# Kernel tuning notes

Hardware: AMD Instinct MI355X
Metric: run time of the kernel (lower is better)

Reference implementation:

```python
import jax, jax.numpy as jnp
import numpy as np

EPS = 1e-6        # RMSNorm epsilon (LLaMA convention)
THETA = 10000.0   # RoPE base, from eqx.nn.RotaryPositionalEmbedding(head_dim, 10000)


def rms_norm(x, w):
    # x: [seq, d]; w: [d]
    var = jnp.mean(x * x, axis=-1, keepdims=True)
    return x * jax.lax.rsqrt(var + EPS) * w


def rope(x, offset):
    # x: [seq, heads, head_dim]; half-split (NeoX/equinox) rotation
    seq, _, hd = x.shape
    half = hd // 2
    inv_freq = 1.0 / (THETA ** (jnp.arange(0, half, dtype=jnp.float32) * 2.0 / hd))
    pos = jnp.arange(seq, dtype=jnp.float32) + offset
    ang = jnp.outer(pos, inv_freq)              # [seq, half]
    cos = jnp.cos(ang)[:, None, :]              # [seq, 1, half]
    sin = jnp.sin(ang)[:, None, :]
    x1, x2 = x[..., :half], x[..., half:]
    return jnp.concatenate([x1 * cos - x2 * sin, x2 * cos + x1 * sin], axis=-1)


def setup_inputs() -> dict:
    D, H, HD, S, C = 4096, 32, 128, 1024, 2048
    ks = jax.random.split(jax.random.key(0), 7)
    sc = 1.0 / np.sqrt(D).astype(np.float32)
    return {
        "xs": jax.random.normal(ks[0], (S, D), jnp.float32),
        "cache_k": jax.random.normal(ks[1], (C, H, HD), jnp.float32),
        "cache_v": jax.random.normal(ks[2], (C, H, HD), jnp.float32),
        "norm_w": jnp.ones((D,), jnp.float32),
        "wq": jax.random.normal(ks[3], (D, D), jnp.float32) * sc,
        "wk": jax.random.normal(ks[4], (D, D), jnp.float32) * sc,
        "wv": jax.random.normal(ks[5], (D, D), jnp.float32) * sc,
        "wo": jax.random.normal(ks[6], (D, D), jnp.float32) * sc,
    }


def reference(xs, cache_k, cache_v, norm_w, wq, wk, wv, wo):
    S, D = xs.shape
    C, H, HD = cache_k.shape
    xn = rms_norm(xs, norm_w)                                   # [S, D]
    # eqx.nn.Linear stores weight as [out, in]: y = x @ W.T
    q = rope((xn @ wq.T).reshape(S, H, HD), C)                  # [S, H, HD]
    k_new = rope((xn @ wk.T).reshape(S, H, HD), C)
    v_new = (xn @ wv.T).reshape(S, H, HD)
    k = jnp.concatenate([cache_k, k_new], axis=0)               # [C+S, H, HD]
    v = jnp.concatenate([cache_v, v_new], axis=0)
    scores = jnp.einsum('shd,thd->hst', q, k) / np.float32(np.sqrt(HD))
    # causal with KV cache: query i (global pos C+i) attends keys j <= C+i
    mask = jnp.arange(C + S)[None, :] <= (jnp.arange(S)[:, None] + C)
    scores = jnp.where(mask[None, :, :], scores, jnp.float32(-1e30))
    probs = jax.nn.softmax(scores, axis=-1)                     # [H, S, C+S]
    attn = jnp.einsum('hst,thd->shd', probs, v).reshape(S, D)
    return attn @ wo.T                                          # [S, D]
```

## Files before the change

kernel.cpp:

```cpp
#include <hip/hip_runtime.h>
#include <cmath>

#define S_LEN 1024
#define D_DIM 4096
#define H_NUM 32
#define HD_DIM 128
#define C_LEN 2048
#define T_LEN 3072

using u16 = unsigned short;
typedef __bf16 bf16x8 __attribute__((ext_vector_type(8)));
typedef float f32x4 __attribute__((ext_vector_type(4)));

__device__ __forceinline__ u16 f2bf(float f) {
  unsigned u = __float_as_uint(f);
  return (u16)((u + 0x7FFFu + ((u >> 16) & 1u)) >> 16);
}

__device__ __forceinline__ f32x4 mfma16(bf16x8 a, bf16x8 b, f32x4 c) {
  return __builtin_amdgcn_mfma_f32_16x16x32_bf16(a, b, c, 0, 0, 0);
}

__device__ __forceinline__ void async_cp16(const u16* g, u16* l) {
  __builtin_amdgcn_global_load_lds((const __attribute__((address_space(1))) unsigned int*)g,
                                   (__attribute__((address_space(3))) unsigned int*)l,
                                   16, 0, 0);
}

__global__ __launch_bounds__(256) void cvt_w4(const float* __restrict__ w0, const float* __restrict__ w1,
                                              const float* __restrict__ w2, const float* __restrict__ w3,
                                              u16* __restrict__ dst) {
  int y = blockIdx.y;
  const float* src = (y == 0) ? w0 : (y == 1) ? w1 : (y == 2) ? w2 : w3;
  int i = blockIdx.x * 256 + threadIdx.x;
  float4 v = ((const float4*)src)[i];
  ushort4 o;
  o.x = f2bf(v.x); o.y = f2bf(v.y); o.z = f2bf(v.z); o.w = f2bf(v.w);
  ((ushort4*)(dst + (size_t)y * D_DIM * D_DIM))[i] = o;
}

__global__ __launch_bounds__(256) void rmsnorm_k(const float* __restrict__ xs, const float* __restrict__ w,
                                                 u16* __restrict__ xn) {
  int row = blockIdx.x, tid = threadIdx.x;
  const float* xr = xs + (size_t)row * D_DIM;
  float4 xv[4];
  float ss = 0.f;
#pragma unroll
  for (int g = 0; g < 4; ++g) {
    xv[g] = *(const float4*)(xr + g * 1024 + tid * 4);
    ss += xv[g].x * xv[g].x + xv[g].y * xv[g].y + xv[g].z * xv[g].z + xv[g].w * xv[g].w;
  }
#pragma unroll
  for (int m = 1; m < 64; m <<= 1) ss += __shfl_xor(ss, m);
  __shared__ float red[4];
  if ((tid & 63) == 0) red[tid >> 6] = ss;
  __syncthreads();
  float rs = rsqrtf((red[0] + red[1] + red[2] + red[3]) * (1.f / D_DIM) + 1e-6f);
  u16* xo = xn + (size_t)row * D_DIM;
#pragma unroll
  for (int g = 0; g < 4; ++g) {
    float4 wv = *(const float4*)(w + g * 1024 + tid * 4);
    ushort4 o;
    o.x = f2bf(xv[g].x * rs * wv.x);
    o.y = f2bf(xv[g].y * rs * wv.y);
    o.z = f2bf(xv[g].z * rs * wv.z);
    o.w = f2bf(xv[g].w * rs * wv.w);
    *(ushort4*)(xo + g * 1024 + tid * 4) = o;
  }
}

__global__ __launch_bounds__(256) void gemm_bt(const u16* __restrict__ A,
                                               const u16* __restrict__ B0, const u16* __restrict__ B1,
                                               const u16* __restrict__ B2,
                                               float* __restrict__ C0, float* __restrict__ C1,
                                               float* __restrict__ C2) {
  __shared__ u16 As[2 * 128 * 32];
  __shared__ u16 Bs[2 * 128 * 32];
  int tid = threadIdx.x;
  int wave = tid >> 6, lane = tid & 63, quad = lane >> 4, l15 = lane & 15;
  int wm = wave >> 1, wn = wave & 1;
  int m0 = blockIdx.y * 128, n0 = blockIdx.x * 128;
  int bz = blockIdx.z;
  const u16* Bp = (bz == 0) ? B0 : ((bz == 1) ? B1 : B2);
  float* Cp = (bz == 0) ? C0 : ((bz == 1) ? C1 : C2);

  f32x4 acc[4][4];
  const f32x4 zero4 = {0.f, 0.f, 0.f, 0.f};
#pragma unroll
  for (int mt = 0; mt < 4; ++mt)
#pragma unroll
    for (int nt = 0; nt < 4; ++nt) acc[mt][nt] = zero4;

  int ar = tid >> 2, acol = (tid & 3) * 8;
  const u16* ga0 = A + (size_t)(m0 + ar) * D_DIM + acol;
  const u16* ga1 = A + (size_t)(m0 + 64 + ar) * D_DIM + acol;
  const u16* gb0 = Bp + (size_t)(n0 + ar) * D_DIM + acol;
  const u16* gb1 = Bp + (size_t)(n0 + 64 + ar) * D_DIM + acol;

  for (int k0 = 0; k0 < D_DIM; k0 += 64) {
    __syncthreads();
#pragma unroll
    for (int hf = 0; hf < 2; ++hf) {
      async_cp16(ga0 + k0 + hf * 32, As + hf * 4096 + (wave << 9));
      async_cp16(ga1 + k0 + hf * 32, As + hf * 4096 + 2048 + (wave << 9));
      async_cp16(gb0 + k0 + hf * 32, Bs + hf * 4096 + (wave << 9));
      async_cp16(gb1 + k0 + hf * 32, Bs + hf * 4096 + 2048 + (wave << 9));
    }
    asm volatile("s_waitcnt vmcnt(0)" ::: "memory");
    __syncthreads();
#pragma unroll
    for (int hf = 0; hf < 2; ++hf) {
      bf16x8 af[4], bfr[4];
#pragma unroll
      for (int mt = 0; mt < 4; ++mt)
        af[mt] = *(const bf16x8*)(As + hf * 4096 + (wm * 64 + mt * 16 + l15) * 32 + quad * 8);
#pragma unroll
      for (int nt = 0; nt < 4; ++nt)
        bfr[nt] = *(const bf16x8*)(Bs + hf * 4096 + (wn * 64 + nt * 16 + l15) * 32 + quad * 8);
#pragma unroll
      for (int mt = 0; mt < 4; ++mt)
#pragma unroll
        for (int nt = 0; nt < 4; ++nt) acc[mt][nt] = mfma16(af[mt], bfr[nt], acc[mt][nt]);
    }
  }
#pragma unroll
  for (int mt = 0; mt < 4; ++mt)
#pragma unroll
    for (int nt = 0; nt < 4; ++nt) {
      int col = n0 + wn * 64 + nt * 16 + l15;
#pragma unroll
      for (int r = 0; r < 4; ++r) {
        int rowm = m0 + wm * 64 + mt * 16 + quad * 4 + r;
        Cp[(size_t)rowm * D_DIM + col] = acc[mt][nt][r];
      }
    }
}

__global__ __launch_bounds__(256) void rope_qk(const float* __restrict__ qlin, const float* __restrict__ klin,
                                               u16* __restrict__ qbf, u16* __restrict__ kc) {
  int part = blockIdx.y;
  int idx = blockIdx.x * 256 + threadIdx.x;
  int i = idx & 63, h = (idx >> 6) & 31, s = idx >> 11;
  size_t base = (size_t)s * D_DIM + h * HD_DIM + i;
  float invf = expf((float)i * -0.14391156831212790f);
  float ang = (float)(s + C_LEN) * invf;
  float sn, cs;
  sincosf(ang, &sn, &cs);
  if (part == 0) {
    float x1 = qlin[base], x2 = qlin[base + 64];
    const float sc = 0.08838834764831845f;
    qbf[base] = f2bf((x1 * cs - x2 * sn) * sc);
    qbf[base + 64] = f2bf((x2 * cs + x1 * sn) * sc);
  } else {
    float x1 = klin[base], x2 = klin[base + 64];
    size_t ob = ((size_t)h * T_LEN + C_LEN + s) * HD_DIM + i;
    kc[ob] = f2bf(x1 * cs - x2 * sn);
    kc[ob + 64] = f2bf(x2 * cs + x1 * sn);
  }
}

__global__ __launch_bounds__(256) void cvt_ck(const float* __restrict__ ck, u16* __restrict__ kc) {
  int idx = blockIdx.x * 256 + threadIdx.x;
  int flat = idx * 4;
  int c = flat >> 12, h = (flat >> 7) & 31, hd = flat & 127;
  float4 v = *(const float4*)(ck + flat);
  ushort4 o;
  o.x = f2bf(v.x); o.y = f2bf(v.y); o.z = f2bf(v.z); o.w = f2bf(v.w);
  *(ushort4*)(kc + ((size_t)h * T_LEN + c) * HD_DIM + hd) = o;
}

__global__ __launch_bounds__(256) void trans_v2(const float* __restrict__ cv, const float* __restrict__ vl,
                                                u16* __restrict__ vt) {
  int h = blockIdx.z, d0 = blockIdx.x * 64, r0 = blockIdx.y * 64;
  const float* src;
  int srow;
  if (r0 < C_LEN) { src = cv; srow = r0; } else { src = vl; srow = r0 - C_LEN; }
  __shared__ float tile[64][65];
  int tid = threadIdx.x;
  int rr = tid >> 4, c4 = (tid & 15) * 4;
#pragma unroll
  for (int p = 0; p < 4; ++p) {
    int r = p * 16 + rr;
    float4 v = *(const float4*)(src + (size_t)(srow + r) * D_DIM + h * HD_DIM + d0 + c4);
    tile[r][c4] = v.x; tile[r][c4 + 1] = v.y; tile[r][c4 + 2] = v.z; tile[r][c4 + 3] = v.w;
  }
  __syncthreads();
#pragma unroll
  for (int p = 0; p < 4; ++p) {
    int dl = p * 16 + rr;
    ushort4 o;
    o.x = f2bf(tile[c4 + 0][dl]);
    o.y = f2bf(tile[c4 + 1][dl]);
    o.z = f2bf(tile[c4 + 2][dl]);
    o.w = f2bf(tile[c4 + 3][dl]);
    *(ushort4*)(vt + ((size_t)h * HD_DIM + d0 + dl) * T_LEN + r0 + c4) = o;
  }
}

__global__ __launch_bounds__(256) void attn_k(const u16* __restrict__ qb, const u16* __restrict__ kc,
                                              const u16* __restrict__ vt, u16* __restrict__ ob) {
  __shared__ u16 Kb[2][8192];
  __shared__ u16 Vb[2][8192];
  int qt = blockIdx.x, h = blockIdx.y;
  int tid = threadIdx.x, wave = tid >> 6, lane = tid & 63, quad = lane >> 4, l15 = lane & 15;

  int qrow = qt * 64 + wave * 16 + l15;
  bf16x8 qf[4];
#pragma unroll
  for (int kt = 0; kt < 4; ++kt)
    qf[kt] = *(const bf16x8*)(qb + (size_t)qrow * D_DIM + h * HD_DIM + kt * 32 + quad * 8);

  f32x4 O[8];
  const f32x4 zero4 = {0.f, 0.f, 0.f, 0.f};
#pragma unroll
  for (int i = 0; i < 8; ++i) O[i] = zero4;
  float mrun[4] = {-INFINITY, -INFINITY, -INFINITY, -INFINITY};
  float lrun[4] = {0.f, 0.f, 0.f, 0.f};

  int kr = tid >> 4;
  int kcg = (tid & 15) ^ (kr & 15);
  int vr = tid >> 3;
  int vcg = (tid & 7) ^ (vr & 7);
  const u16* kg = kc + ((size_t)h * T_LEN + kr) * HD_DIM + kcg * 8;
  const u16* vg = vt + ((size_t)h * HD_DIM + vr) * T_LEN + vcg * 8;

  auto stage = [&](int kb, int buf) {
    const u16* kp = kg + (size_t)kb * 64 * HD_DIM;
    const u16* vp = vg + (size_t)kb * 64;
#pragma unroll
    for (int p = 0; p < 4; ++p) async_cp16(kp + p * 16 * HD_DIM, &Kb[buf][p * 2048 + (wave << 9)]);
#pragma unroll
    for (int p = 0; p < 4; ++p) async_cp16(vp + (size_t)p * 32 * T_LEN, &Vb[buf][p * 2048 + (wave << 9)]);
  };

  stage(0, 0);
  int nkb = 33 + qt;
  for (int kb = 0; kb < nkb; ++kb) {
    int cur = kb & 1;
    asm volatile("s_waitcnt vmcnt(0)" ::: "memory");
    __syncthreads();
    if (kb + 1 < nkb) stage(kb + 1, cur ^ 1);

    f32x4 sc4[4];
#pragma unroll
    for (int nt = 0; nt < 4; ++nt) {
      f32x4 s = zero4;
#pragma unroll
      for (int kt = 0; kt < 4; ++kt) {
        int row = nt * 16 + l15;
        bf16x8 bv = *(const bf16x8*)&Kb[cur][row * 128 + (((kt * 4 + quad) ^ l15) * 8)];
        s = mfma16(qf[kt], bv, s);
      }
      sc4[nt] = s;
    }
    if (kb == nkb - 1) {
#pragma unroll
      for (int nt = 0; nt < 4; ++nt) {
        int t = kb * 64 + nt * 16 + l15;
#pragma unroll
        for (int r = 0; r < 4; ++r) {
          int srow = qt * 64 + wave * 16 + quad * 4 + r;
          if (t > C_LEN + srow) sc4[nt][r] = -INFINITY;
        }
      }
    }
    float alpha4[4];
#pragma unroll
    for (int r = 0; r < 4; ++r) {
      float mx = fmaxf(fmaxf(sc4[0][r], sc4[1][r]), fmaxf(sc4[2][r], sc4[3][r]));
      mx = fmaxf(mx, __shfl_xor(mx, 1));
      mx = fmaxf(mx, __shfl_xor(mx, 2));
      mx = fmaxf(mx, __shfl_xor(mx, 4));
      mx = fmaxf(mx, __shfl_xor(mx, 8));
      float nm = fmaxf(mrun[r], mx);
      float al = __expf(mrun[r] - nm);
      float ps = 0.f;
#pragma unroll
      for (int nt = 0; nt < 4; ++nt) {
        float p = __expf(sc4[nt][r] - nm);
        sc4[nt][r] = p;
        ps += p;
      }
      ps += __shfl_xor(ps, 1);
      ps += __shfl_xor(ps, 2);
      ps += __shfl_xor(ps, 4);
      ps += __shfl_xor(ps, 8);
      lrun[r] = lrun[r] * al + ps;
      mrun[r] = nm;
      alpha4[r] = al;
    }
#pragma unroll
    for (int i = 0; i < 8; ++i)
#pragma unroll
      for (int r = 0; r < 4; ++r) O[i][r] *= alpha4[r];

    asm volatile("s_waitcnt lgkmcnt(0)\n\ts_barrier" ::: "memory");

    u16* pw = &Kb[cur][wave * 1152];
#pragma unroll
    for (int nt = 0; nt < 4; ++nt)
#pragma unroll
      for (int r = 0; r < 4; ++r)
        pw[(quad * 4 + r) * 72 + nt * 16 + l15] = f2bf(sc4[nt][r]);
    asm volatile("s_waitcnt lgkmcnt(0)" ::: "memory");

#pragma unroll
    for (int kt2 = 0; kt2 < 2; ++kt2) {
      bf16x8 af = *(const bf16x8*)(pw + l15 * 72 + kt2 * 32 + quad * 8);
#pragma unroll
      for (int nt2 = 0; nt2 < 8; ++nt2) {
        int row = nt2 * 16 + l15;
        bf16x8 bv = *(const bf16x8*)&Vb[cur][row * 64 + (((kt2 * 4 + quad) ^ (l15 & 7)) * 8)];
        O[nt2] = mfma16(af, bv, O[nt2]);
      }
    }
  }
  float inv[4];
#pragma unroll
  for (int r = 0; r < 4; ++r) inv[r] = 1.f / lrun[r];
#pragma unroll
  for (int nt2 = 0; nt2 < 8; ++nt2)
#pragma unroll
    for (int r = 0; r < 4; ++r) {
      int srow = qt * 64 + wave * 16 + quad * 4 + r;
      ob[(size_t)srow * D_DIM + h * HD_DIM + nt2 * 16 + l15] = f2bf(O[nt2][r] * inv[r]);
    }
}

extern "C" void kernel_launch(void* const* d_in, const int* in_sizes, int n_in,
                              void* d_out, int out_size, void* d_ws, size_t ws_size,
                              hipStream_t stream) {
  const float* xs = (const float*)d_in[0];
  const float* cache_k = (const float*)d_in[1];
  const float* cache_v = (const float*)d_in[2];
  const float* norm_w = (const float*)d_in[3];
  const float* wq = (const float*)d_in[4];
  const float* wk = (const float*)d_in[5];
  const float* wv = (const float*)d_in[6];
  const float* wo = (const float*)d_in[7];
  float* out = (float*)d_out;

  char* ws = (char*)d_ws;
  size_t off = 0;
  auto take = [&](size_t b) -> void* {
    char* p = ws + off;
    off += (b + 255) & ~(size_t)255;
    return (void*)p;
  };
  u16* w_bf = (u16*)take((size_t)4 * D_DIM * D_DIM * 2);
  u16* wq_bf = w_bf;
  u16* wk_bf = w_bf + (size_t)D_DIM * D_DIM;
  u16* wv_bf = w_bf + (size_t)2 * D_DIM * D_DIM;
  u16* wo_bf = w_bf + (size_t)3 * D_DIM * D_DIM;
  u16* xn_bf = (u16*)take((size_t)S_LEN * D_DIM * 2);
  float* q_lin = (float*)take((size_t)S_LEN * D_DIM * 4);
  float* k_lin = (float*)take((size_t)S_LEN * D_DIM * 4);
  float* v_lin = (float*)take((size_t)S_LEN * D_DIM * 4);
  u16* q_bf = (u16*)take((size_t)S_LEN * D_DIM * 2);
  u16* k_cat = (u16*)take((size_t)H_NUM * T_LEN * HD_DIM * 2);
  u16* v_t = (u16*)take((size_t)H_NUM * T_LEN * HD_DIM * 2);
  u16* attn_bf = (u16*)take((size_t)S_LEN * D_DIM * 2);

  cvt_w4<<<dim3(D_DIM * D_DIM / 4 / 256, 4), 256, 0, stream>>>(wq, wk, wv, wo, w_bf);
  rmsnorm_k<<<S_LEN, 256, 0, stream>>>(xs, norm_w, xn_bf);
  gemm_bt<<<dim3(32, 8, 3), 256, 0, stream>>>(xn_bf, wq_bf, wk_bf, wv_bf, q_lin, k_lin, v_lin);
  rope_qk<<<dim3((S_LEN * H_NUM * 64) / 256, 2), 256, 0, stream>>>(q_lin, k_lin, q_bf, k_cat);
  cvt_ck<<<(C_LEN * H_NUM * HD_DIM / 4) / 256, 256, 0, stream>>>(cache_k, k_cat);
  trans_v2<<<dim3(2, T_LEN / 64, H_NUM), 256, 0, stream>>>(cache_v, v_lin, v_t);
  attn_k<<<dim3(16, 32), 256, 0, stream>>>(q_bf, k_cat, v_t, attn_bf);
  gemm_bt<<<dim3(32, 8, 1), 256, 0, stream>>>(attn_bf, wo_bf, wo_bf, wo_bf, out, out, out);
}
```

Baseline: 734.4 us.

## Triple-buffer GEMM LDS loads with swizzled layout to overlap copies and compute

Replaces the single-stage load-then-compute loop in the projection GEMM with a three-stage ring of 32-wide K tiles. Async global-to-LDS copies are issued two iterations ahead and gated with partial vmcnt waits, so memory traffic overlaps MFMA work. It also XOR-swizzles the 16-byte column chunks on both the store and read sides to reduce LDS bank conflicts. In exchange it uses more LDS per block and needs two barriers per smaller K step.

Result: faster. 716.6 us (-2.4%).

```diff
diff --git a/kernel.cpp b/kernel.cpp
--- a/kernel.cpp
+++ b/kernel.cpp
@@ -74,8 +74,8 @@
                                                const u16* __restrict__ B2,
                                                float* __restrict__ C0, float* __restrict__ C1,
                                                float* __restrict__ C2) {
-  __shared__ u16 As[2 * 128 * 32];
-  __shared__ u16 Bs[2 * 128 * 32];
+  __shared__ u16 As[3 * 4096];
+  __shared__ u16 Bs[3 * 4096];
   int tid = threadIdx.x;
   int wave = tid >> 6, lane = tid & 63, quad = lane >> 4, l15 = lane & 15;
   int wm = wave >> 1, wn = wave & 1;
@@ -91,37 +91,51 @@
 #pragma unroll
     for (int nt = 0; nt < 4; ++nt) acc[mt][nt] = zero4;
 
-  int ar = tid >> 2, acol = (tid & 3) * 8;
-  const u16* ga0 = A + (size_t)(m0 + ar) * D_DIM + acol;
-  const u16* ga1 = A + (size_t)(m0 + 64 + ar) * D_DIM + acol;
-  const u16* gb0 = Bp + (size_t)(n0 + ar) * D_DIM + acol;
-  const u16* gb1 = Bp + (size_t)(n0 + 64 + ar) * D_DIM + acol;
-
-  for (int k0 = 0; k0 < D_DIM; k0 += 64) {
-    __syncthreads();
-#pragma unroll
-    for (int hf = 0; hf < 2; ++hf) {
-      async_cp16(ga0 + k0 + hf * 32, As + hf * 4096 + (wave << 9));
-      async_cp16(ga1 + k0 + hf * 32, As + hf * 4096 + 2048 + (wave << 9));
-      async_cp16(gb0 + k0 + hf * 32, Bs + hf * 4096 + (wave << 9));
-      async_cp16(gb1 + k0 + hf * 32, Bs + hf * 4096 + 2048 + (wave << 9));
-    }
-    asm volatile("s_waitcnt vmcnt(0)" ::: "memory");
-    __syncthreads();
-#pragma unroll
-    for (int hf = 0; hf < 2; ++hf) {
-      bf16x8 af[4], bfr[4];
-#pragma unroll
-      for (int mt = 0; mt < 4; ++mt)
-        af[mt] = *(const bf16x8*)(As + hf * 4096 + (wm * 64 + mt * 16 + l15) * 32 + quad * 8);
-#pragma unroll
-      for (int nt = 0; nt < 4; ++nt)
-        bfr[nt] = *(const bf16x8*)(Bs + hf * 4096 + (wn * 64 + nt * 16 + l15) * 32 + quad * 8);
-#pragma unroll
-      for (int mt = 0; mt < 4; ++mt)
-#pragma unroll
-        for (int nt = 0; nt < 4; ++nt) acc[mt][nt] = mfma16(af[mt], bfr[nt], acc[mt][nt]);
-    }
+  int ar = tid >> 2;
+  int acs = ((tid & 3) ^ ((tid >> 3) & 3)) * 8;
+  const u16* ga0 = A + (size_t)(m0 + ar) * D_DIM + acs;
+  const u16* ga1 = A + (size_t)(m0 + 64 + ar) * D_DIM + acs;
+  const u16* gb0 = Bp + (size_t)(n0 + ar) * D_DIM + acs;
+  const u16* gb1 = Bp + (size_t)(n0 + 64 + ar) * D_DIM + acs;
+
+  auto stage = [&](int k0, int s) {
+    async_cp16(ga0 + k0, As + s * 4096 + (wave << 9));
+    async_cp16(ga1 + k0, As + s * 4096 + 2048 + (wave << 9));
+    async_cp16(gb0 + k0, Bs + s * 4096 + (wave << 9));
+    async_cp16(gb1 + k0, Bs + s * 4096 + 2048 + (wave << 9));
+  };
+
+  stage(0, 0);
+  stage(32, 1);
+  int buf = 0;
+  int sw = (quad ^ ((l15 >> 1) & 3)) * 8;
+  const int NIT = D_DIM / 32;
+  for (int it = 0; it < NIT; ++it) {
+    if (it + 2 < NIT) {
+      int nb = buf + 2; if (nb >= 3) nb -= 3;
+      stage((it + 2) * 32, nb);
+      asm volatile("s_waitcnt vmcnt(8)" ::: "memory");
+    } else if (it + 1 < NIT) {
+      asm volatile("s_waitcnt vmcnt(4)" ::: "memory");
+    } else {
+      asm volatile("s_waitcnt vmcnt(0)" ::: "memory");
+    }
+    asm volatile("s_barrier" ::: "memory");
+    const u16* Ab = As + buf * 4096;
+    const u16* Bb = Bs + buf * 4096;
+    bf16x8 af[4], bfr[4];
+#pragma unroll
+    for (int mt = 0; mt < 4; ++mt)
+      af[mt] = *(const bf16x8*)(Ab + (wm * 64 + mt * 16 + l15) * 32 + sw);
+#pragma unroll
+    for (int nt = 0; nt < 4; ++nt)
+      bfr[nt] = *(const bf16x8*)(Bb + (wn * 64 + nt * 16 + l15) * 32 + sw);
+#pragma unroll
+    for (int mt = 0; mt < 4; ++mt)
+#pragma unroll
+      for (int nt = 0; nt < 4; ++nt) acc[mt][nt] = mfma16(af[mt], bfr[nt], acc[mt][nt]);
+    asm volatile("s_waitcnt lgkmcnt(0)\n\ts_barrier" ::: "memory");
+    if (++buf == 3) buf = 0;
   }
 #pragma unroll
   for (int mt = 0; mt < 4; ++mt)
```
